# Kernel tuning notes

Measured on AMD Instinct MI355X. Metric: run time of the kernel, lower is better.

## Reference

```python
import jax, jax.numpy as jnp
import numpy as np

N, E, C, H, M = 10000, 160000, 512, 512, 2000  # nodes, edges, in=out ch, hidden ch, missing nodes


def setup_inputs() -> dict:
    key = jax.random.key(0)
    ks = jax.random.split(key, 9)
    s = 0.05  # weight init scale
    x = jax.random.normal(ks[0], (N, C), dtype=jnp.float32)
    edge_index = jax.random.randint(ks[1], (2, E), 0, N, dtype=jnp.int32)
    W1 = jax.random.normal(ks[2], (C, H), dtype=jnp.float32) * s
    b1 = jnp.zeros((H,), dtype=jnp.float32)
    W2 = jax.random.normal(ks[3], (H, H), dtype=jnp.float32) * s
    b2 = jnp.zeros((H,), dtype=jnp.float32)
    W3 = jax.random.normal(ks[4], (H, C), dtype=jnp.float32) * s
    b3 = jnp.zeros((C,), dtype=jnp.float32)
    noise = jax.random.normal(ks[5], (M, H), dtype=jnp.float32)  # stands in for torch.randn in forward
    return {"x": x, "edge_index": edge_index, "W1": W1, "b1": b1, "W2": W2,
            "b2": b2, "W3": W3, "b3": b3, "noise": noise, "num_missing_nodes": M}


def reference(x, edge_index, W1, b1, W2, b2, W3, b3, noise, num_missing_nodes):
    n = x.shape[0]
    loops = jnp.arange(n, dtype=edge_index.dtype)
    src = jnp.concatenate([edge_index[0], loops])  # add self-loops (PyG GCNConv default)
    dst = jnp.concatenate([edge_index[1], loops])
    deg = jax.ops.segment_sum(jnp.ones_like(dst, x.dtype), dst, num_segments=n)
    dis = jnp.where(deg > 0, jax.lax.rsqrt(jnp.maximum(deg, 1.0)), 0.0)
    norm = dis[src] * dis[dst]  # [E+N]

    def gcn(h, W, b):
        h = h @ W                              # linear (no bias) before aggregation
        msg = norm[:, None] * h[src]           # gather + normalize
        return jax.ops.segment_sum(msg, dst, num_segments=n) + b  # scatter-add + bias

    h = jax.nn.relu(gcn(x, W1, b1))
    h = jax.nn.relu(gcn(h, W2, b2))
    pred = noise @ W3 + b3                     # [M, C]
    return jnp.concatenate([h, pred], axis=0)  # [N+M, C] (requires H == C)
```

## Files before the change

### kernel.cpp

```cpp
#include <hip/hip_runtime.h>
#include <hip/hip_bf16.h>

typedef __attribute__((ext_vector_type(8))) short short8;
typedef __attribute__((ext_vector_type(8))) unsigned short ushort8v;
typedef __attribute__((ext_vector_type(4))) float f32x4;

#define CDIM 512
#define SLOTS 64

__device__ __forceinline__ float bf2f(unsigned short u) {
    union { unsigned int i; float f; } w; w.i = ((unsigned int)u) << 16; return w.f;
}
__device__ __forceinline__ unsigned short f2bf(float f) {
    __bf16 b = (__bf16)f;
    union { __bf16 b; unsigned short u; } w; w.b = b;
    return w.u;
}

__device__ __forceinline__ void decode_bxby(int b, int nbA, int& bx, int& by) {
    int nfull = (nbA >> 3) << 5;
    if (b < nfull) {
        int sup = b >> 5, loc = b & 31;
        bx = sup * 8 + (loc & 7);
        by = loc >> 3;
    } else {
        int bb = b - nfull;
        bx = ((nbA >> 3) << 3) + (bb >> 2);
        by = bb & 3;
    }
}

__global__ __launch_bounds__(256) void prep_kernel(
    const float* __restrict__ W1, const float* __restrict__ W2,
    const float* __restrict__ W3,
    unsigned short* __restrict__ W1t, unsigned short* __restrict__ W2t,
    unsigned short* __restrict__ W3t,
    int* __restrict__ cursor, int n) {
    int b = blockIdx.x;
    if (b < 192) {
        int w = b >> 6;
        const float* s = (w == 0) ? W1 : (w == 1) ? W2 : W3;
        unsigned short* d = (w == 0) ? W1t : (w == 1) ? W2t : W3t;
        int tb = b & 63;
        int k0 = (tb >> 3) << 6, n0 = (tb & 7) << 6;
        __shared__ unsigned short ld[64][66];
        int t = threadIdx.x;
        {
            int kk = t >> 2, nseg = (t & 3) * 16;
            const float4* sp = (const float4*)(s + (size_t)(k0 + kk) * 512 + n0 + nseg);
            float4 f0 = sp[0], f1 = sp[1], f2 = sp[2], f3 = sp[3];
            unsigned short* lp = &ld[kk][nseg];
            lp[0] = f2bf(f0.x);  lp[1] = f2bf(f0.y);  lp[2] = f2bf(f0.z);  lp[3] = f2bf(f0.w);
            lp[4] = f2bf(f1.x);  lp[5] = f2bf(f1.y);  lp[6] = f2bf(f1.z);  lp[7] = f2bf(f1.w);
            lp[8] = f2bf(f2.x);  lp[9] = f2bf(f2.y);  lp[10] = f2bf(f2.z); lp[11] = f2bf(f2.w);
            lp[12] = f2bf(f3.x); lp[13] = f2bf(f3.y); lp[14] = f2bf(f3.z); lp[15] = f2bf(f3.w);
        }
        __syncthreads();
        {
            int nn = t >> 2, kseg = (t & 3) * 16;
            ushort8v o0, o1;
#pragma unroll
            for (int i = 0; i < 8; i++) { o0[i] = ld[kseg + i][nn]; o1[i] = ld[kseg + 8 + i][nn]; }
            unsigned short* dp = d + (size_t)(n0 + nn) * 512 + k0 + kseg;
            *(ushort8v*)(dp) = o0;
            *(ushort8v*)(dp + 8) = o1;
        }
    } else {
        int i = (b - 192) * 256 + threadIdx.x;
        if (i < n) cursor[i] = 0;
    }
}

template <int AF32, int MODE>
__device__ __forceinline__ void gemm_block64(
    const float* __restrict__ Af, const unsigned short* __restrict__ Ab,
    const unsigned short* __restrict__ Bt, const float* __restrict__ bias,
    const int* __restrict__ cnt,
    unsigned short* __restrict__ outb, float* __restrict__ outf,
    int Mrows, int bx, int by)
{
    const int K = 512;
    __shared__ unsigned short As[64][72];
    __shared__ unsigned short Bs[128][72];

    int t = threadIdx.x;
    int lane = t & 63;
    int wid = t >> 6;
    int wm = wid >> 1, wn = wid & 1;
    int m0 = bx * 64;
    int n0 = by * 128;

    f32x4 acc[2][4];
#pragma unroll
    for (int i = 0; i < 2; i++)
#pragma unroll
        for (int j = 0; j < 4; j++) acc[i][j] = (f32x4){0.f, 0.f, 0.f, 0.f};

    int arow = t >> 2;
    int aseg = (t & 3) * 16;
    int brow = t >> 1;
    int bseg = (t & 1) * 32;
    int agr = m0 + arow;
    bool aok = (agr < Mrows);

    ushort8v ra[2];
    ushort8v rb[4];

    auto loadA = [&](int k0) {
        if (aok) {
            if (AF32) {
                const float4* ap = (const float4*)(Af + (size_t)agr * K + k0 + aseg);
                float4 f0 = ap[0], f1 = ap[1], f2 = ap[2], f3 = ap[3];
                ra[0][0] = f2bf(f0.x); ra[0][1] = f2bf(f0.y); ra[0][2] = f2bf(f0.z); ra[0][3] = f2bf(f0.w);
                ra[0][4] = f2bf(f1.x); ra[0][5] = f2bf(f1.y); ra[0][6] = f2bf(f1.z); ra[0][7] = f2bf(f1.w);
                ra[1][0] = f2bf(f2.x); ra[1][1] = f2bf(f2.y); ra[1][2] = f2bf(f2.z); ra[1][3] = f2bf(f2.w);
                ra[1][4] = f2bf(f3.x); ra[1][5] = f2bf(f3.y); ra[1][6] = f2bf(f3.z); ra[1][7] = f2bf(f3.w);
            } else {
                const ushort8v* ap = (const ushort8v*)(Ab + (size_t)agr * K + k0 + aseg);
                ra[0] = ap[0]; ra[1] = ap[1];
            }
        } else {
            ushort8v z = (ushort8v){0,0,0,0,0,0,0,0};
            ra[0] = z; ra[1] = z;
        }
    };
    auto loadB = [&](int k0) {
        const ushort8v* bp = (const ushort8v*)(Bt + (size_t)(n0 + brow) * K + k0 + bseg);
        rb[0] = bp[0]; rb[1] = bp[1]; rb[2] = bp[2]; rb[3] = bp[3];
    };
    auto storeAB = [&]() {
        *(ushort8v*)&As[arow][aseg + 0] = ra[0];
        *(ushort8v*)&As[arow][aseg + 8] = ra[1];
        *(ushort8v*)&Bs[brow][bseg + 0]  = rb[0];
        *(ushort8v*)&Bs[brow][bseg + 8]  = rb[1];
        *(ushort8v*)&Bs[brow][bseg + 16] = rb[2];
        *(ushort8v*)&Bs[brow][bseg + 24] = rb[3];
    };

    loadA(0); loadB(0); storeAB();
    __syncthreads();

    for (int k0 = 0; k0 < K; k0 += 64) {
        bool more = (k0 + 64 < K);
        if (more) { loadA(k0 + 64); loadB(k0 + 64); }

#pragma unroll
        for (int ks = 0; ks < 64; ks += 32) {
            short8 af[2], bf[4];
            int kk = ks + 8 * (lane >> 4);
            int rbase = wm * 32 + (lane & 15);
            int cbase = wn * 64 + (lane & 15);
#pragma unroll
            for (int fm = 0; fm < 2; fm++) af[fm] = *(const short8*)&As[rbase + fm * 16][kk];
#pragma unroll
            for (int fn = 0; fn < 4; fn++) bf[fn] = *(const short8*)&Bs[cbase + fn * 16][kk];
#pragma unroll
            for (int fm = 0; fm < 2; fm++)
#pragma unroll
                for (int fn = 0; fn < 4; fn++)
                    acc[fm][fn] = __builtin_amdgcn_mfma_f32_16x16x32_bf16(af[fm], bf[fn], acc[fm][fn], 0, 0, 0);
        }
        __syncthreads();
        if (more) {
            storeAB();
            __syncthreads();
        }
    }

    int rl = (lane >> 4) * 4;
    int cc = lane & 15;
#pragma unroll
    for (int fm = 0; fm < 2; fm++) {
#pragma unroll
        for (int r = 0; r < 4; r++) {
            int row = m0 + wm * 32 + fm * 16 + rl + r;
            if (row >= Mrows) continue;
            float dv = (MODE == 2) ? rsqrtf((float)(cnt[row] + 1)) : 1.f;
#pragma unroll
            for (int fn = 0; fn < 4; fn++) {
                int col = n0 + wn * 64 + fn * 16 + cc;
                float v = acc[fm][fn][r];
                if (MODE == 1) {
                    __builtin_nontemporal_store(v + bias[col], outf + (size_t)row * CDIM + col);
                } else if (MODE == 2) {
                    outb[(size_t)row * CDIM + col] = f2bf(dv * v);
                } else {
                    outb[(size_t)row * CDIM + col] = f2bf(v);
                }
            }
        }
    }
}

__global__ __launch_bounds__(256) void gemm1_pred_fill_kernel(
    const float* __restrict__ x, const unsigned short* __restrict__ W1t,
    unsigned short* __restrict__ t0,
    const float* __restrict__ noise, const unsigned short* __restrict__ W3t,
    const float* __restrict__ b3, float* __restrict__ out_pred,
    const int* __restrict__ esrc, const int* __restrict__ edst,
    int* __restrict__ cursor, int* __restrict__ cols,
    int N, int M, int E, int nbA, int nbP)
{
    int b = blockIdx.x;
    int nbG = nbA * 4, nbP4 = nbP * 4;
    if (b < nbG) {
        int bx, by; decode_bxby(b, nbA, bx, by);
        gemm_block64<1, 3>(x, nullptr, W1t, nullptr, nullptr, t0, nullptr, N, bx, by);
    } else if (b < nbG + nbP4) {
        int bx, by; decode_bxby(b - nbG, nbP, bx, by);
        gemm_block64<1, 1>(noise, nullptr, W3t, b3, nullptr, nullptr, out_pred, M, bx, by);
    } else {
        int i = (b - nbG - nbP4) * 256 + threadIdx.x;
        if (i < E) {
            int d = edst[i];
            int pos = atomicAdd(&cursor[d], 1);
            if (pos < SLOTS) cols[(d << 6) + pos] = esrc[i];
        }
    }
}

__global__ __launch_bounds__(256) void gemm2_kernel(
    const unsigned short* __restrict__ h1, const unsigned short* __restrict__ W2t,
    const int* __restrict__ counts, unsigned short* __restrict__ t1, int N, int nbA)
{
    int bx, by; decode_bxby(blockIdx.x, nbA, bx, by);
    gemm_block64<0, 2>(nullptr, h1, W2t, nullptr, counts, t1, nullptr, N, bx, by);
}

template <int SRCW, int OUTF32>
__global__ __launch_bounds__(256) void aggregate_kernel(
    const unsigned short* __restrict__ t,
    const int* __restrict__ counts, const int* __restrict__ cols,
    const float* __restrict__ bias,
    unsigned short* __restrict__ outb, float* __restrict__ outf, int n)
{
    int gw = (blockIdx.x * 256 + threadIdx.x) >> 6;
    if (gw >= n) return;
    int lane = threadIdx.x & 63;
    int cbase = lane * 8;

    int deg = min(counts[gw], SLOTS);
    float di = rsqrtf((float)(counts[gw] + 1));
    ushort8v v = *(const ushort8v*)(t + (size_t)gw * CDIM + cbase);
    float acc[8];
    float selfw = SRCW ? di : 1.f;
#pragma unroll
    for (int j = 0; j < 8; j++) acc[j] = selfw * bf2f(v[j]);

    const int* cp = cols + ((size_t)gw << 6);
    int s = 0;
    for (; s + 4 <= deg; s += 4) {
        int s0 = cp[s], s1 = cp[s + 1], s2 = cp[s + 2], s3 = cp[s + 3];
        float w0 = 1.f, w1 = 1.f, w2 = 1.f, w3 = 1.f;
        if (SRCW) {
            w0 = rsqrtf((float)(counts[s0] + 1));
            w1 = rsqrtf((float)(counts[s1] + 1));
            w2 = rsqrtf((float)(counts[s2] + 1));
            w3 = rsqrtf((float)(counts[s3] + 1));
        }
        ushort8v u0 = *(const ushort8v*)(t + (size_t)s0 * CDIM + cbase);
        ushort8v u1 = *(const ushort8v*)(t + (size_t)s1 * CDIM + cbase);
        ushort8v u2 = *(const ushort8v*)(t + (size_t)s2 * CDIM + cbase);
        ushort8v u3 = *(const ushort8v*)(t + (size_t)s3 * CDIM + cbase);
#pragma unroll
        for (int j = 0; j < 8; j++) {
            if (SRCW)
                acc[j] += (w0 * bf2f(u0[j]) + w1 * bf2f(u1[j])) + (w2 * bf2f(u2[j]) + w3 * bf2f(u3[j]));
            else
                acc[j] += (bf2f(u0[j]) + bf2f(u1[j])) + (bf2f(u2[j]) + bf2f(u3[j]));
        }
    }
    for (; s < deg; ++s) {
        int src = cp[s];
        float w = SRCW ? rsqrtf((float)(counts[src] + 1)) : 1.f;
        ushort8v u = *(const ushort8v*)(t + (size_t)src * CDIM + cbase);
#pragma unroll
        for (int j = 0; j < 8; j++) acc[j] += w * bf2f(u[j]);
    }

    if (OUTF32) {
        float* op = outf + (size_t)gw * CDIM + cbase;
#pragma unroll
        for (int j = 0; j < 8; j++)
            __builtin_nontemporal_store(fmaxf(di * acc[j] + bias[cbase + j], 0.f), op + j);
    } else {
        ushort8v o;
#pragma unroll
        for (int j = 0; j < 8; j++) {
            float t2 = fmaxf(di * acc[j] + bias[cbase + j], 0.f);
            o[j] = f2bf(t2);
        }
        *(ushort8v*)(outb + (size_t)gw * CDIM + cbase) = o;
    }
}

extern "C" void kernel_launch(void* const* d_in, const int* in_sizes, int n_in,
                              void* d_out, int out_size, void* d_ws, size_t ws_size,
                              hipStream_t stream) {
    const float* x     = (const float*)d_in[0];
    const int*   ei    = (const int*)d_in[1];
    const float* W1    = (const float*)d_in[2];
    const float* b1    = (const float*)d_in[3];
    const float* W2    = (const float*)d_in[4];
    const float* b2    = (const float*)d_in[5];
    const float* W3    = (const float*)d_in[6];
    const float* b3    = (const float*)d_in[7];
    const float* noise = (const float*)d_in[8];

    const int N = in_sizes[0] / CDIM;
    const int E = in_sizes[1] / 2;
    const int M = in_sizes[8] / CDIM;
    const int* esrc = ei;
    const int* edst = ei + E;

    char* ws = (char*)d_ws;
    size_t off = 0;
    auto alloc = [&](size_t bytes) -> void* {
        void* p = ws + off;
        off += (bytes + 255) & ~(size_t)255;
        return p;
    };
    unsigned short* W1t = (unsigned short*)alloc(512 * 512 * 2);
    unsigned short* W2t = (unsigned short*)alloc(512 * 512 * 2);
    unsigned short* W3t = (unsigned short*)alloc(512 * 512 * 2);
    unsigned short* t0  = (unsigned short*)alloc((size_t)N * CDIM * 2);
    unsigned short* h1b = (unsigned short*)alloc((size_t)N * CDIM * 2);
    int*   cursor = (int*)alloc((size_t)N * 4);
    int*   cols   = (int*)alloc((size_t)N * SLOTS * 4);

    float* out_h    = (float*)d_out;
    float* out_pred = (float*)d_out + (size_t)N * CDIM;

    const int nbA = (N + 63) / 64;
    const int nbP = (M + 63) / 64;
    const int ZB  = (N + 255) / 256;
    const int FB  = (E + 255) / 256;
    const int nbG = nbA * 4, nbP4 = nbP * 4;

    prep_kernel<<<192 + ZB, 256, 0, stream>>>(W1, W2, W3, W1t, W2t, W3t, cursor, N);
    gemm1_pred_fill_kernel<<<nbG + nbP4 + FB, 256, 0, stream>>>(
        x, W1t, t0, noise, W3t, b3, out_pred, esrc, edst, cursor, cols,
        N, M, E, nbA, nbP);
    int agg_blocks = (N + 3) / 4;
    aggregate_kernel<1, 0><<<agg_blocks, 256, 0, stream>>>(t0, cursor, cols, b1, h1b, nullptr, N);
    gemm2_kernel<<<nbG, 256, 0, stream>>>(h1b, W2t, cursor, t0, N, nbA);
    aggregate_kernel<0, 1><<<agg_blocks, 256, 0, stream>>>(t0, cursor, cols, b2, nullptr, out_h, N);
}
```

Before: 99.27 us.

## Use 128x128 GEMM tiles with direct global-to-LDS loads and pre-converted bf16 inputs

Pre-converts x and noise to bf16 in the prep kernel, enlarges GEMM tiles from 64x128 to 128x128 per block, and loads A/B tiles straight into LDS with global_load_lds instead of staging through registers. The aim is more MFMA work per loaded byte and fewer instructions in the load path. In exchange it drops register double-buffering, so loads and compute no longer overlap. It also removes the LDS padding, which may bring bank conflicts, and adds a full bf16 conversion pass plus padded buffers. Rows past N/M are read from padded workspace that is not zeroed, but those rows are masked on output.

```diff
diff --git a/kernel.cpp b/kernel.cpp
--- a/kernel.cpp
+++ b/kernel.cpp
@@ -4,6 +4,7 @@
 typedef __attribute__((ext_vector_type(8))) short short8;
 typedef __attribute__((ext_vector_type(8))) unsigned short ushort8v;
 typedef __attribute__((ext_vector_type(4))) float f32x4;
+typedef unsigned int u32;
 
 #define CDIM 512
 #define SLOTS 64
@@ -15,6 +16,12 @@
     __bf16 b = (__bf16)f;
     union { __bf16 b; unsigned short u; } w; w.b = b;
     return w.u;
+}
+
+__device__ __forceinline__ void gload_lds16(const unsigned short* g, unsigned short* l) {
+    __builtin_amdgcn_global_load_lds(
+        (const __attribute__((address_space(1))) u32*)g,
+        (__attribute__((address_space(3))) u32*)l, 16, 0, 0);
 }
 
 __device__ __forceinline__ void decode_bxby(int b, int nbA, int& bx, int& by) {
@@ -35,8 +42,12 @@
     const float* __restrict__ W3,
     unsigned short* __restrict__ W1t, unsigned short* __restrict__ W2t,
     unsigned short* __restrict__ W3t,
-    int* __restrict__ cursor, int n) {
+    int* __restrict__ cursor, int n,
+    const float* __restrict__ x, unsigned short* __restrict__ xb,
+    const float* __restrict__ noise, unsigned short* __restrict__ noiseb,
+    int ZB, int CXB, int CNB) {
     int b = blockIdx.x;
+    int t = threadIdx.x;
     if (b < 192) {
         int w = b >> 6;
         const float* s = (w == 0) ? W1 : (w == 1) ? W2 : W3;
@@ -44,7 +55,6 @@
         int tb = b & 63;
         int k0 = (tb >> 3) << 6, n0 = (tb & 7) << 6;
         __shared__ unsigned short ld[64][66];
-        int t = threadIdx.x;
         {
             int kk = t >> 2, nseg = (t & 3) * 16;
             const float4* sp = (const float4*)(s + (size_t)(k0 + kk) * 512 + n0 + nseg);
@@ -65,115 +75,91 @@
             *(ushort8v*)(dp) = o0;
             *(ushort8v*)(dp + 8) = o1;
         }
-    } else {
-        int i = (b - 192) * 256 + threadIdx.x;
+        return;
+    }
+    b -= 192;
+    if (b < ZB) {
+        int i = b * 256 + t;
         if (i < n) cursor[i] = 0;
-    }
-}
-
-template <int AF32, int MODE>
-__device__ __forceinline__ void gemm_block64(
-    const float* __restrict__ Af, const unsigned short* __restrict__ Ab,
-    const unsigned short* __restrict__ Bt, const float* __restrict__ bias,
-    const int* __restrict__ cnt,
+        return;
+    }
+    b -= ZB;
+    const float* s; unsigned short* d;
+    if (b < CXB) { s = x; d = xb; }
+    else { b -= CXB; s = noise; d = noiseb; }
+    int i = b * 256 + t;
+    const float4* sp = (const float4*)(s + (size_t)i * 8);
+    float4 a0 = sp[0], a1 = sp[1];
+    ushort8v o;
+    o[0] = f2bf(a0.x); o[1] = f2bf(a0.y); o[2] = f2bf(a0.z); o[3] = f2bf(a0.w);
+    o[4] = f2bf(a1.x); o[5] = f2bf(a1.y); o[6] = f2bf(a1.z); o[7] = f2bf(a1.w);
+    *(ushort8v*)(d + (size_t)i * 8) = o;
+}
+
+template <int MODE>
+__device__ __forceinline__ void gemm_block128(
+    const unsigned short* __restrict__ Ab,
+    const unsigned short* __restrict__ Bt,
+    const float* __restrict__ bias, const int* __restrict__ cnt,
     unsigned short* __restrict__ outb, float* __restrict__ outf,
     int Mrows, int bx, int by)
 {
     const int K = 512;
-    __shared__ unsigned short As[64][72];
-    __shared__ unsigned short Bs[128][72];
+    __shared__ unsigned short As[128 * 64];
+    __shared__ unsigned short Bs[128 * 64];
 
     int t = threadIdx.x;
     int lane = t & 63;
     int wid = t >> 6;
     int wm = wid >> 1, wn = wid & 1;
-    int m0 = bx * 64;
+    int m0 = bx * 128;
     int n0 = by * 128;
 
-    f32x4 acc[2][4];
-#pragma unroll
-    for (int i = 0; i < 2; i++)
+    f32x4 acc[4][4];
+#pragma unroll
+    for (int i = 0; i < 4; i++)
 #pragma unroll
         for (int j = 0; j < 4; j++) acc[i][j] = (f32x4){0.f, 0.f, 0.f, 0.f};
 
-    int arow = t >> 2;
-    int aseg = (t & 3) * 16;
-    int brow = t >> 1;
-    int bseg = (t & 1) * 32;
-    int agr = m0 + arow;
-    bool aok = (agr < Mrows);
-
-    ushort8v ra[2];
-    ushort8v rb[4];
-
-    auto loadA = [&](int k0) {
-        if (aok) {
-            if (AF32) {
-                const float4* ap = (const float4*)(Af + (size_t)agr * K + k0 + aseg);
-                float4 f0 = ap[0], f1 = ap[1], f2 = ap[2], f3 = ap[3];
-                ra[0][0] = f2bf(f0.x); ra[0][1] = f2bf(f0.y); ra[0][2] = f2bf(f0.z); ra[0][3] = f2bf(f0.w);
-                ra[0][4] = f2bf(f1.x); ra[0][5] = f2bf(f1.y); ra[0][6] = f2bf(f1.z); ra[0][7] = f2bf(f1.w);
-                ra[1][0] = f2bf(f2.x); ra[1][1] = f2bf(f2.y); ra[1][2] = f2bf(f2.z); ra[1][3] = f2bf(f2.w);
-                ra[1][4] = f2bf(f3.x); ra[1][5] = f2bf(f3.y); ra[1][6] = f2bf(f3.z); ra[1][7] = f2bf(f3.w);
-            } else {
-                const ushort8v* ap = (const ushort8v*)(Ab + (size_t)agr * K + k0 + aseg);
-                ra[0] = ap[0]; ra[1] = ap[1];
-            }
-        } else {
-            ushort8v z = (ushort8v){0,0,0,0,0,0,0,0};
-            ra[0] = z; ra[1] = z;
-        }
-    };
-    auto loadB = [&](int k0) {
-        const ushort8v* bp = (const ushort8v*)(Bt + (size_t)(n0 + brow) * K + k0 + bseg);
-        rb[0] = bp[0]; rb[1] = bp[1]; rb[2] = bp[2]; rb[3] = bp[3];
-    };
-    auto storeAB = [&]() {
-        *(ushort8v*)&As[arow][aseg + 0] = ra[0];
-        *(ushort8v*)&As[arow][aseg + 8] = ra[1];
-        *(ushort8v*)&Bs[brow][bseg + 0]  = rb[0];
-        *(ushort8v*)&Bs[brow][bseg + 8]  = rb[1];
-        *(ushort8v*)&Bs[brow][bseg + 16] = rb[2];
-        *(ushort8v*)&Bs[brow][bseg + 24] = rb[3];
-    };
-
-    loadA(0); loadB(0); storeAB();
-    __syncthreads();
+    int lrow = lane >> 3;
+    int kseg = (lane & 7) * 8;
 
     for (int k0 = 0; k0 < K; k0 += 64) {
-        bool more = (k0 + 64 < K);
-        if (more) { loadA(k0 + 64); loadB(k0 + 64); }
+#pragma unroll
+        for (int i = 0; i < 4; i++) {
+            int chunk = i * 4 + wid;
+            int row = chunk * 8 + lrow;
+            gload_lds16(Ab + (size_t)(m0 + row) * K + k0 + kseg, As + chunk * 512);
+            gload_lds16(Bt + (size_t)(n0 + row) * K + k0 + kseg, Bs + chunk * 512);
+        }
+        __syncthreads();
 
 #pragma unroll
         for (int ks = 0; ks < 64; ks += 32) {
-            short8 af[2], bf[4];
+            short8 af[4], bf[4];
             int kk = ks + 8 * (lane >> 4);
-            int rbase = wm * 32 + (lane & 15);
+            int rbase = wm * 64 + (lane & 15);
             int cbase = wn * 64 + (lane & 15);
 #pragma unroll
-            for (int fm = 0; fm < 2; fm++) af[fm] = *(const short8*)&As[rbase + fm * 16][kk];
-#pragma unroll
-            for (int fn = 0; fn < 4; fn++) bf[fn] = *(const short8*)&Bs[cbase + fn * 16][kk];
-#pragma unroll
-            for (int fm = 0; fm < 2; fm++)
+            for (int fm = 0; fm < 4; fm++) af[fm] = *(const short8*)&As[(rbase + fm * 16) * 64 + kk];
+#pragma unroll
+            for (int fn = 0; fn < 4; fn++) bf[fn] = *(const short8*)&Bs[(cbase + fn * 16) * 64 + kk];
+#pragma unroll
+            for (int fm = 0; fm < 4; fm++)
 #pragma unroll
                 for (int fn = 0; fn < 4; fn++)
                     acc[fm][fn] = __builtin_amdgcn_mfma_f32_16x16x32_bf16(af[fm], bf[fn], acc[fm][fn], 0, 0, 0);
         }
         __syncthreads();
-        if (more) {
-            storeAB();
-            __syncthreads();
-        }
     }
 
     int rl = (lane >> 4) * 4;
     int cc = lane & 15;
 #pragma unroll
-    for (int fm = 0; fm < 2; fm++) {
+    for (int fm = 0; fm < 4; fm++) {
 #pragma unroll
         for (int r = 0; r < 4; r++) {
-            int row = m0 + wm * 32 + fm * 16 + rl + r;
+            int row = m0 + wm * 64 + fm * 16 + rl + r;
             if (row >= Mrows) continue;
             float dv = (MODE == 2) ? rsqrtf((float)(cnt[row] + 1)) : 1.f;
 #pragma unroll
@@ -193,9 +179,9 @@
 }
 
 __global__ __launch_bounds__(256) void gemm1_pred_fill_kernel(
-    const float* __restrict__ x, const unsigned short* __restrict__ W1t,
+    const unsigned short* __restrict__ xb, const unsigned short* __restrict__ W1t,
     unsigned short* __restrict__ t0,
-    const float* __restrict__ noise, const unsigned short* __restrict__ W3t,
+    const unsigned short* __restrict__ noiseb, const unsigned short* __restrict__ W3t,
     const float* __restrict__ b3, float* __restrict__ out_pred,
     const int* __restrict__ esrc, const int* __restrict__ edst,
     int* __restrict__ cursor, int* __restrict__ cols,
@@ -205,10 +191,10 @@
     int nbG = nbA * 4, nbP4 = nbP * 4;
     if (b < nbG) {
         int bx, by; decode_bxby(b, nbA, bx, by);
-        gemm_block64<1, 3>(x, nullptr, W1t, nullptr, nullptr, t0, nullptr, N, bx, by);
+        gemm_block128<3>(xb, W1t, nullptr, nullptr, t0, nullptr, N, bx, by);
     } else if (b < nbG + nbP4) {
         int bx, by; decode_bxby(b - nbG, nbP, bx, by);
-        gemm_block64<1, 1>(noise, nullptr, W3t, b3, nullptr, nullptr, out_pred, M, bx, by);
+        gemm_block128<1>(noiseb, W3t, b3, nullptr, nullptr, out_pred, M, bx, by);
     } else {
         int i = (b - nbG - nbP4) * 256 + threadIdx.x;
         if (i < E) {
@@ -224,7 +210,7 @@
     const int* __restrict__ counts, unsigned short* __restrict__ t1, int N, int nbA)
 {
     int bx, by; decode_bxby(blockIdx.x, nbA, bx, by);
-    gemm_block64<0, 2>(nullptr, h1, W2t, nullptr, counts, t1, nullptr, N, bx, by);
+    gemm_block128<2>(h1, W2t, nullptr, counts, t1, nullptr, N, bx, by);
 }
 
 template <int SRCW, int OUTF32>
@@ -313,6 +299,11 @@
     const int* esrc = ei;
     const int* edst = ei + E;
 
+    const int nbA = (N + 127) / 128;
+    const int nbP = (M + 127) / 128;
+    const int Nr  = nbA * 128;
+    const int Mr  = nbP * 128;
+
     char* ws = (char*)d_ws;
     size_t off = 0;
     auto alloc = [&](size_t bytes) -> void* {
@@ -320,26 +311,29 @@
         off += (bytes + 255) & ~(size_t)255;
         return p;
     };
-    unsigned short* W1t = (unsigned short*)alloc(512 * 512 * 2);
-    unsigned short* W2t = (unsigned short*)alloc(512 * 512 * 2);
-    unsigned short* W3t = (unsigned short*)alloc(512 * 512 * 2);
-    unsigned short* t0  = (unsigned short*)alloc((size_t)N * CDIM * 2);
-    unsigned short* h1b = (unsigned short*)alloc((size_t)N * CDIM * 2);
+    unsigned short* W1t    = (unsigned short*)alloc(512 * 512 * 2);
+    unsigned short* W2t    = (unsigned short*)alloc(512 * 512 * 2);
+    unsigned short* W3t    = (unsigned short*)alloc(512 * 512 * 2);
+    unsigned short* xb     = (unsigned short*)alloc((size_t)Nr * CDIM * 2);
+    unsigned short* noiseb = (unsigned short*)alloc((size_t)Mr * CDIM * 2);
+    unsigned short* t0     = (unsigned short*)alloc((size_t)N * CDIM * 2);
+    unsigned short* h1b    = (unsigned short*)alloc((size_t)Nr * CDIM * 2);
     int*   cursor = (int*)alloc((size_t)N * 4);
     int*   cols   = (int*)alloc((size_t)N * SLOTS * 4);
 
     float* out_h    = (float*)d_out;
     float* out_pred = (float*)d_out + (size_t)N * CDIM;
 
-    const int nbA = (N + 63) / 64;
-    const int nbP = (M + 63) / 64;
     const int ZB  = (N + 255) / 256;
+    const int CXB = (N * CDIM / 8) / 256;
+    const int CNB = (M * CDIM / 8) / 256;
     const int FB  = (E + 255) / 256;
     const int nbG = nbA * 4, nbP4 = nbP * 4;
 
-    prep_kernel<<<192 + ZB, 256, 0, stream>>>(W1, W2, W3, W1t, W2t, W3t, cursor, N);
+    prep_kernel<<<192 + ZB + CXB + CNB, 256, 0, stream>>>(
+        W1, W2, W3, W1t, W2t, W3t, cursor, N, x, xb, noise, noiseb, ZB, CXB, CNB);
     gemm1_pred_fill_kernel<<<nbG + nbP4 + FB, 256, 0, stream>>>(
-        x, W1t, t0, noise, W3t, b3, out_pred, esrc, edst, cursor, cols,
+        xb, W1t, t0, noiseb, W3t, b3, out_pred, esrc, edst, cursor, cols,
         N, M, E, nbA, nbP);
     int agg_blocks = (N + 3) / 4;
     aggregate_kernel<1, 0><<<agg_blocks, 256, 0, stream>>>(t0, cursor, cols, b1, h1b, nullptr, N);
```

After: 95.57 us. -3.7%, faster.
